# Optimization experiments

Measured on AMD Instinct MI355X. Metric: run time of the kernel, lower is better.

## Reference

```python
import jax, jax.numpy as jnp
import numpy as np

DIM = 1024
HEADS = 8
HEAD_DIM = DIM // HEADS


def setup_inputs() -> dict:
    key = jax.random.key(0)
    k1, k2, k3, k4 = jax.random.split(key, 4)
    x = jax.random.normal(k1, (4, 4096, DIM), dtype=jnp.float32)
    # torch nn.Linear(dim, 3*dim, bias=False): stored here as [in, out]
    W_qkv = jax.random.normal(k2, (DIM, 3 * DIM), dtype=jnp.float32) * (1.0 / np.sqrt(DIM))
    W_out = jax.random.normal(k3, (DIM, DIM), dtype=jnp.float32) * (1.0 / np.sqrt(DIM))
    b_out = jax.random.normal(k4, (DIM,), dtype=jnp.float32) * 0.01
    return {"x": x, "W_qkv": W_qkv, "W_out": W_out, "b_out": b_out}


def reference(x, W_qkv, W_out, b_out):
    b, n, _ = x.shape
    qkv = x @ W_qkv                                   # [b, n, 3*dim]
    q, k, v = jnp.split(qkv, 3, axis=-1)
    # [b, n, dim] -> [b, h, n, d]
    split_heads = lambda t: t.reshape(b, n, HEADS, HEAD_DIM).transpose(0, 2, 1, 3)
    q = jax.nn.sigmoid(split_heads(q))
    k = jnp.tanh(split_heads(k))
    v = split_heads(v)
    # linear attention: kv = k^T @ v  -> [b, h, d, d]
    kv = jnp.einsum('bhnd,bhne->bhde', k, v)
    out = jnp.einsum('bhnd,bhde->bhne', q, kv)        # [b, h, n, d]
    out = out.transpose(0, 2, 1, 3).reshape(b, n, DIM)
    return out @ W_out + b_out
```

## Files before the change

kernel.cpp:

```cpp
#include <hip/hip_runtime.h>
#include <hip/hip_bf16.h>
#include <math.h>

typedef __attribute__((ext_vector_type(4))) float f32x4;
typedef __attribute__((ext_vector_type(8))) __bf16 bf16x8;
typedef unsigned short u16;
typedef __attribute__((ext_vector_type(4))) u16 u16x4;
typedef __attribute__((ext_vector_type(8))) u16 u16x8;

#define NTOK 16384
#define SEQ  4096

__device__ __forceinline__ void gload16(void* lds, const void* g) {
    __builtin_amdgcn_global_load_lds(
        (const __attribute__((address_space(1))) unsigned int*)g,
        (__attribute__((address_space(3))) unsigned int*)lds, 16, 0, 0);
}

__device__ __forceinline__ int xcd_swizzle(int bid, int nwg) {
    int cpx = nwg >> 3;
    return (bid & 7) * cpx + (bid >> 3);
}

__global__ void cast_x_kernel(const float* __restrict__ in, __bf16* __restrict__ out, int n) {
    int stride = gridDim.x * blockDim.x * 8;
    for (int i = (blockIdx.x * blockDim.x + threadIdx.x) * 8; i < n; i += stride) {
        f32x4 v0 = *(const f32x4*)(in + i);
        f32x4 v1 = *(const f32x4*)(in + i + 4);
        u16x8 pk;
        pk[0] = __builtin_bit_cast(u16, (__bf16)v0.x);
        pk[1] = __builtin_bit_cast(u16, (__bf16)v0.y);
        pk[2] = __builtin_bit_cast(u16, (__bf16)v0.z);
        pk[3] = __builtin_bit_cast(u16, (__bf16)v0.w);
        pk[4] = __builtin_bit_cast(u16, (__bf16)v1.x);
        pk[5] = __builtin_bit_cast(u16, (__bf16)v1.y);
        pk[6] = __builtin_bit_cast(u16, (__bf16)v1.z);
        pk[7] = __builtin_bit_cast(u16, (__bf16)v1.w);
        *(u16x8*)(out + i) = pk;
    }
}

__global__ void transpose_cast(const float* __restrict__ in, __bf16* __restrict__ out,
                               int R, int C) {
    __shared__ float t[32][33];
    int bx = blockIdx.x * 32;
    int by = blockIdx.y * 32;
    int tx = threadIdx.x & 31, ty = threadIdx.x >> 5;
    #pragma unroll
    for (int j = 0; j < 32; j += 8)
        t[ty + j][tx] = in[(size_t)(by + ty + j) * C + bx + tx];
    __syncthreads();
    #pragma unroll
    for (int j = 0; j < 32; j += 8)
        out[(size_t)(bx + ty + j) * R + by + tx] = (__bf16)t[tx][ty + j];
}

__launch_bounds__(256)
__global__ void qkv_gemm(const __bf16* __restrict__ X,
                         const __bf16* __restrict__ WT,
                         __bf16* __restrict__ Q,
                         __bf16* __restrict__ KT,
                         __bf16* __restrict__ VT) {
    __shared__ __bf16 As[128 * 64];
    __shared__ __bf16 Bs[128 * 64];
    const int swz = xcd_swizzle(blockIdx.x, 128 * 24);
    const int mblk = swz & 127;
    const int nblk = swz >> 7;
    const int tid = threadIdx.x;
    const int lane = tid & 63;
    const int wave = tid >> 6;
    const int wr = wave >> 1, wc = wave & 1;
    const int mBase = mblk * 128, nBase = nblk * 128;

    f32x4 acc[4][4] = {};

    for (int kt = 0; kt < 16; ++kt) {
        const int k0 = kt * 64;
        #pragma unroll
        for (int it = 0; it < 4; ++it) {
            int slot = it * 256 + tid;
            int r = slot >> 3, cs = slot & 7;
            int cg = cs ^ (r & 7);
            gload16((char*)As + slot * 16, X + (size_t)(mBase + r) * 1024 + k0 + cg * 8);
        }
        #pragma unroll
        for (int it = 0; it < 4; ++it) {
            int slot = it * 256 + tid;
            int r = slot >> 3, cs = slot & 7;
            int cg = cs ^ (r & 7);
            gload16((char*)Bs + slot * 16, WT + (size_t)(nBase + r) * 1024 + k0 + cg * 8);
        }
        __syncthreads();
        #pragma unroll
        for (int kk = 0; kk < 2; ++kk) {
            bf16x8 a[4], b[4];
            const int kb = kk * 4 + (lane >> 4);
            #pragma unroll
            for (int m = 0; m < 4; ++m) {
                int row = wr * 64 + m * 16 + (lane & 15);
                a[m] = *(const bf16x8*)((const char*)As + row * 128 + (kb ^ (row & 7)) * 16);
            }
            #pragma unroll
            for (int n = 0; n < 4; ++n) {
                int row = wc * 64 + n * 16 + (lane & 15);
                b[n] = *(const bf16x8*)((const char*)Bs + row * 128 + (kb ^ (row & 7)) * 16);
            }
            #pragma unroll
            for (int m = 0; m < 4; ++m)
                #pragma unroll
                for (int n = 0; n < 4; ++n)
                    acc[m][n] = __builtin_amdgcn_mfma_f32_16x16x32_bf16(a[m], b[n], acc[m][n], 0, 0, 0);
        }
        __syncthreads();
    }

    const int sec = nblk >> 3;
    const int head = nblk & 7;
    #pragma unroll
    for (int m = 0; m < 4; ++m) {
        const int row0 = mBase + wr * 64 + m * 16 + (lane >> 4) * 4;
        #pragma unroll
        for (int n = 0; n < 4; ++n) {
            const int col = wc * 64 + n * 16 + (lane & 15);
            if (sec == 0) {
                #pragma unroll
                for (int j = 0; j < 4; ++j) {
                    float v = acc[m][n][j];
                    v = 1.0f / (1.0f + __expf(-v));
                    Q[(size_t)(row0 + j) * 1024 + head * 128 + col] = (__bf16)v;
                }
            } else {
                u16x4 pk;
                #pragma unroll
                for (int j = 0; j < 4; ++j) {
                    float v = acc[m][n][j];
                    if (sec == 1) {
                        float e = __expf(-2.0f * fabsf(v));
                        v = copysignf((1.0f - e) / (1.0f + e), v);
                    }
                    pk[j] = __builtin_bit_cast(u16, (__bf16)v);
                }
                const int b = row0 >> 12, nn = row0 & 4095;
                __bf16* dst = (sec == 1) ? KT : VT;
                *(u16x4*)(dst + ((size_t)(b * 8 + head) * 128 + col) * SEQ + nn) = pk;
            }
        }
    }
}

__launch_bounds__(256)
__global__ void kv_gemm(const __bf16* __restrict__ KT, const __bf16* __restrict__ VT,
                        float* __restrict__ KVp) {
    const int bh = blockIdx.x >> 3;
    const int chunk = blockIdx.x & 7;
    const int tid = threadIdx.x, lane = tid & 63, wave = tid >> 6;
    const int wr = wave >> 1, wc = wave & 1;
    const __bf16* Kb = KT + (size_t)bh * 128 * SEQ;
    const __bf16* Vb = VT + (size_t)bh * 128 * SEQ;
    f32x4 acc[4][4] = {};
    const int nb = chunk * 512 + (lane >> 4) * 8;
    for (int ks = 0; ks < 16; ++ks) {
        const int n0 = nb + ks * 32;
        bf16x8 a[4], b[4];
        #pragma unroll
        for (int m = 0; m < 4; ++m) {
            int d = wr * 64 + m * 16 + (lane & 15);
            a[m] = *(const bf16x8*)(Kb + (size_t)d * SEQ + n0);
        }
        #pragma unroll
        for (int n = 0; n < 4; ++n) {
            int e = wc * 64 + n * 16 + (lane & 15);
            b[n] = *(const bf16x8*)(Vb + (size_t)e * SEQ + n0);
        }
        #pragma unroll
        for (int m = 0; m < 4; ++m)
            #pragma unroll
            for (int n = 0; n < 4; ++n)
                acc[m][n] = __builtin_amdgcn_mfma_f32_16x16x32_bf16(a[m], b[n], acc[m][n], 0, 0, 0);
    }
    float* out = KVp + ((size_t)bh * 8 + chunk) * 16384;
    #pragma unroll
    for (int m = 0; m < 4; ++m) {
        const int r0 = wr * 64 + m * 16 + (lane >> 4) * 4;
        #pragma unroll
        for (int n = 0; n < 4; ++n) {
            const int col = wc * 64 + n * 16 + (lane & 15);
            #pragma unroll
            for (int j = 0; j < 4; ++j)
                out[(r0 + j) * 128 + col] = acc[m][n][j];
        }
    }
}

__launch_bounds__(256)
__global__ void kvw_gemm(const float* __restrict__ KVp, const __bf16* __restrict__ WoT,
                         __bf16* __restrict__ MT) {
    const int bh = blockIdx.x >> 3, ft = blockIdx.x & 7;
    const int b = bh >> 3, h = bh & 7;
    const int tid = threadIdx.x, lane = tid & 63, wave = tid >> 6;
    const int wr = wave >> 1, wc = wave & 1;
    const float* A = KVp + (size_t)bh * 8 * 16384;
    f32x4 acc[4][4] = {};
    for (int ks = 0; ks < 4; ++ks) {
        const int e0 = ks * 32 + (lane >> 4) * 8;
        bf16x8 a[4], bfr[4];
        #pragma unroll
        for (int m = 0; m < 4; ++m) {
            int d = wr * 64 + m * 16 + (lane & 15);
            f32x4 u = {0.f, 0.f, 0.f, 0.f};
            f32x4 w = {0.f, 0.f, 0.f, 0.f};
            #pragma unroll
            for (int c = 0; c < 8; ++c) {
                u += *(const f32x4*)(A + c * 16384 + d * 128 + e0);
                w += *(const f32x4*)(A + c * 16384 + d * 128 + e0 + 4);
            }
            bf16x8 t;
            t[0]=(__bf16)u.x; t[1]=(__bf16)u.y; t[2]=(__bf16)u.z; t[3]=(__bf16)u.w;
            t[4]=(__bf16)w.x; t[5]=(__bf16)w.y; t[6]=(__bf16)w.z; t[7]=(__bf16)w.w;
            a[m] = t;
        }
        #pragma unroll
        for (int n = 0; n < 4; ++n) {
            int f = ft * 128 + wc * 64 + n * 16 + (lane & 15);
            bfr[n] = *(const bf16x8*)(WoT + (size_t)f * 1024 + h * 128 + e0);
        }
        #pragma unroll
        for (int m = 0; m < 4; ++m)
            #pragma unroll
            for (int n = 0; n < 4; ++n)
                acc[m][n] = __builtin_amdgcn_mfma_f32_16x16x32_bf16(a[m], bfr[n], acc[m][n], 0, 0, 0);
    }
    __bf16* MTb = MT + (size_t)b * 1024 * 1024;
    #pragma unroll
    for (int m = 0; m < 4; ++m) {
        const int d0 = wr * 64 + m * 16 + (lane >> 4) * 4;
        #pragma unroll
        for (int n = 0; n < 4; ++n) {
            const int f = ft * 128 + wc * 64 + n * 16 + (lane & 15);
            u16x4 pk;
            #pragma unroll
            for (int j = 0; j < 4; ++j)
                pk[j] = __builtin_bit_cast(u16, (__bf16)acc[m][n][j]);
            *(u16x4*)(MTb + (size_t)f * 1024 + h * 128 + d0) = pk;
        }
    }
}

__launch_bounds__(256)
__global__ void final_gemm(const __bf16* __restrict__ Q,
                           const __bf16* __restrict__ MT,
                           const float* __restrict__ bias,
                           float* __restrict__ out) {
    __shared__ __bf16 As[128 * 64];
    __shared__ __bf16 Bs[128 * 64];
    const int swz = xcd_swizzle(blockIdx.x, 128 * 8);
    const int mblk = swz & 127;
    const int nblk = swz >> 7;
    const int tid = threadIdx.x;
    const int lane = tid & 63;
    const int wave = tid >> 6;
    const int wr = wave >> 1, wc = wave & 1;
    const int mBase = mblk * 128, nBase = nblk * 128;
    const int b = mBase >> 12;
    const __bf16* Bsrc = MT + (size_t)b * 1024 * 1024;

    f32x4 acc[4][4] = {};

    for (int kt = 0; kt < 16; ++kt) {
        const int k0 = kt * 64;
        #pragma unroll
        for (int it = 0; it < 4; ++it) {
            int slot = it * 256 + tid;
            int r = slot >> 3, cs = slot & 7;
            int cg = cs ^ (r & 7);
            gload16((char*)As + slot * 16, Q + (size_t)(mBase + r) * 1024 + k0 + cg * 8);
        }
        #pragma unroll
        for (int it = 0; it < 4; ++it) {
            int slot = it * 256 + tid;
            int r = slot >> 3, cs = slot & 7;
            int cg = cs ^ (r & 7);
            gload16((char*)Bs + slot * 16, Bsrc + (size_t)(nBase + r) * 1024 + k0 + cg * 8);
        }
        __syncthreads();
        #pragma unroll
        for (int kk = 0; kk < 2; ++kk) {
            bf16x8 a[4], bfr[4];
            const int kb = kk * 4 + (lane >> 4);
            #pragma unroll
            for (int m = 0; m < 4; ++m) {
                int row = wr * 64 + m * 16 + (lane & 15);
                a[m] = *(const bf16x8*)((const char*)As + row * 128 + (kb ^ (row & 7)) * 16);
            }
            #pragma unroll
            for (int n = 0; n < 4; ++n) {
                int row = wc * 64 + n * 16 + (lane & 15);
                bfr[n] = *(const bf16x8*)((const char*)Bs + row * 128 + (kb ^ (row & 7)) * 16);
            }
            #pragma unroll
            for (int m = 0; m < 4; ++m)
                #pragma unroll
                for (int n = 0; n < 4; ++n)
                    acc[m][n] = __builtin_amdgcn_mfma_f32_16x16x32_bf16(a[m], bfr[n], acc[m][n], 0, 0, 0);
        }
        __syncthreads();
    }

    #pragma unroll
    for (int m = 0; m < 4; ++m) {
        const int row0 = mBase + wr * 64 + m * 16 + (lane >> 4) * 4;
        #pragma unroll
        for (int n = 0; n < 4; ++n) {
            const int col = nBase + wc * 64 + n * 16 + (lane & 15);
            const float bv = bias[col];
            #pragma unroll
            for (int j = 0; j < 4; ++j)
                out[(size_t)(row0 + j) * 1024 + col] = acc[m][n][j] + bv;
        }
    }
}

extern "C" void kernel_launch(void* const* d_in, const int* in_sizes, int n_in,
                              void* d_out, int out_size, void* d_ws, size_t ws_size,
                              hipStream_t stream) {
    const float* x    = (const float*)d_in[0];
    const float* Wqkv = (const float*)d_in[1];
    const float* Wout = (const float*)d_in[2];
    const float* bout = (const float*)d_in[3];
    float* out = (float*)d_out;
    char* ws = (char*)d_ws;
    char* ob = (char*)d_out;

    __bf16* xb  = (__bf16*)(ob);
    float*  KVp = (float*)(ob + 33554432ull);
    __bf16* wqt = (__bf16*)(ws);
    __bf16* wot = (__bf16*)(ws + 6291456ull);
    __bf16* Q   = (__bf16*)(ws + 8388608ull);
    __bf16* KT  = (__bf16*)(ws + 41943040ull);
    __bf16* VT  = (__bf16*)(ws + 75497472ull);
    __bf16* MT  = (__bf16*)(ws + 109051904ull);

    hipLaunchKernelGGL(cast_x_kernel, dim3(2048), dim3(256), 0, stream, x, xb, NTOK * 1024);
    hipLaunchKernelGGL(transpose_cast, dim3(96, 32), dim3(256), 0, stream, Wqkv, wqt, 1024, 3072);
    hipLaunchKernelGGL(transpose_cast, dim3(32, 32), dim3(256), 0, stream, Wout, wot, 1024, 1024);
    hipLaunchKernelGGL(qkv_gemm, dim3(128 * 24), dim3(256), 0, stream, xb, wqt, Q, KT, VT);
    hipLaunchKernelGGL(kv_gemm, dim3(256), dim3(256), 0, stream, KT, VT, KVp);
    hipLaunchKernelGGL(kvw_gemm, dim3(256), dim3(256), 0, stream, KVp, wot, MT);
    hipLaunchKernelGGL(final_gemm, dim3(128 * 8), dim3(256), 0, stream, Q, MT, bout, out);
}
```

Before: 405.2 us.

## Replace 128x128 GEMMs with pipelined 256x256 eight-wave GEMM kernels

Rewrites the QKV projection and final output GEMMs as 256x256-tile kernels with 8 waves and a 4-stage LDS ring buffer of 32-wide K slices. Global-to-LDS loads are issued ahead and overlap MFMA work through explicit vmcnt waits, barriers, sched_barriers and setprio. The goal is more operand reuse per tile and latency hiding in place of the old load-sync-compute loop. The cost is more registers and LDS per block (one block per CU) and fewer blocks, which can hurt load balance, especially for the 256-block final GEMM.

```diff
diff --git a/kernel.cpp b/kernel.cpp
--- a/kernel.cpp
+++ b/kernel.cpp
@@ -55,95 +55,167 @@
         out[(size_t)(bx + ty + j) * R + by + tx] = (__bf16)t[tx][ty + j];
 }
 
-__launch_bounds__(256)
-__global__ void qkv_gemm(const __bf16* __restrict__ X,
-                         const __bf16* __restrict__ WT,
-                         __bf16* __restrict__ Q,
-                         __bf16* __restrict__ KT,
-                         __bf16* __restrict__ VT) {
-    __shared__ __bf16 As[128 * 64];
-    __shared__ __bf16 Bs[128 * 64];
-    const int swz = xcd_swizzle(blockIdx.x, 128 * 24);
-    const int mblk = swz & 127;
-    const int nblk = swz >> 7;
-    const int tid = threadIdx.x;
-    const int lane = tid & 63;
-    const int wave = tid >> 6;
-    const int wr = wave >> 1, wc = wave & 1;
-    const int mBase = mblk * 128, nBase = nblk * 128;
-
-    f32x4 acc[4][4] = {};
-
-    for (int kt = 0; kt < 16; ++kt) {
-        const int k0 = kt * 64;
-        #pragma unroll
-        for (int it = 0; it < 4; ++it) {
-            int slot = it * 256 + tid;
-            int r = slot >> 3, cs = slot & 7;
-            int cg = cs ^ (r & 7);
-            gload16((char*)As + slot * 16, X + (size_t)(mBase + r) * 1024 + k0 + cg * 8);
-        }
-        #pragma unroll
-        for (int it = 0; it < 4; ++it) {
-            int slot = it * 256 + tid;
-            int r = slot >> 3, cs = slot & 7;
-            int cg = cs ^ (r & 7);
-            gload16((char*)Bs + slot * 16, WT + (size_t)(nBase + r) * 1024 + k0 + cg * 8);
-        }
-        __syncthreads();
-        #pragma unroll
-        for (int kk = 0; kk < 2; ++kk) {
-            bf16x8 a[4], b[4];
-            const int kb = kk * 4 + (lane >> 4);
-            #pragma unroll
-            for (int m = 0; m < 4; ++m) {
-                int row = wr * 64 + m * 16 + (lane & 15);
-                a[m] = *(const bf16x8*)((const char*)As + row * 128 + (kb ^ (row & 7)) * 16);
-            }
-            #pragma unroll
-            for (int n = 0; n < 4; ++n) {
-                int row = wc * 64 + n * 16 + (lane & 15);
-                b[n] = *(const bf16x8*)((const char*)Bs + row * 128 + (kb ^ (row & 7)) * 16);
-            }
-            #pragma unroll
-            for (int m = 0; m < 4; ++m)
-                #pragma unroll
-                for (int n = 0; n < 4; ++n)
-                    acc[m][n] = __builtin_amdgcn_mfma_f32_16x16x32_bf16(a[m], b[n], acc[m][n], 0, 0, 0);
-        }
-        __syncthreads();
-    }
-
-    const int sec = nblk >> 3;
-    const int head = nblk & 7;
-    #pragma unroll
-    for (int m = 0; m < 4; ++m) {
-        const int row0 = mBase + wr * 64 + m * 16 + (lane >> 4) * 4;
-        #pragma unroll
-        for (int n = 0; n < 4; ++n) {
-            const int col = wc * 64 + n * 16 + (lane & 15);
+
+#define PHASE(p)                                                                     \
+    {                                                                                \
+        constexpr int cs = (p) >> 1;                      \
+        constexpr int nh = (p) & 1;                                      \
+        constexpr int ss = (((p) >> 1) + 3) & 3;            \
+        if constexpr (nh == 0) {                \
+            const char* ab = (const char*)AL + cs * 16384;                           \
+            _Pragma("unroll")                                                        \
+            for (int m = 0; m < 8; ++m)                                              \
+                a[m] = *(const bf16x8*)(ab + aoff0 + m * 1024);                      \
+        }                                                                            \
+        bf16x8 b0, b1;                                                               \
+        {                                                                            \
+            const char* bb = (const char*)BL + cs * 16384;                           \
+            b0 = *(const bf16x8*)(bb + boff0 + (nh * 2 + 0) * 1024);                 \
+            b1 = *(const bf16x8*)(bb + boff0 + (nh * 2 + 1) * 1024);                 \
+        }                                                                            \
+        {      \
+            const int n = 4 * itr + ((p) >> 1) + 3;                                  \
+            const int ns = n < 32 ? n : 31;                   \
+            if constexpr (((p) & 1) == 0) {                                          \
+                char* dst = (char*)AL + ss * 16384;                                  \
+                gload16(dst + fb0, Asrc + ael0 + ns * 32);                           \
+                gload16(dst + fb1, Asrc + ael1 + ns * 32);                           \
+            } else {                                                                 \
+                char* dst = (char*)BL + ss * 16384;                                  \
+                gload16(dst + fb0, Bsrc + bel0 + ns * 32);                           \
+                gload16(dst + fb1, Bsrc + bel1 + ns * 32);                           \
+            }                                                                        \
+        }                                                                            \
+        if constexpr (((p) & 3) == 3) {                                              \
+            asm volatile("s_waitcnt vmcnt(4)" ::: "memory");                         \
+            __builtin_amdgcn_sched_barrier(0);                                       \
+        }                                                                            \
+        __builtin_amdgcn_s_barrier();                                                \
+        __builtin_amdgcn_sched_barrier(0);                                           \
+        __builtin_amdgcn_s_setprio(1);                                               \
+        _Pragma("unroll")                                                            \
+        for (int m = 0; m < 8; ++m) {                                                \
+            acc[m][nh * 2 + 0] = __builtin_amdgcn_mfma_f32_16x16x32_bf16(            \
+                a[m], b0, acc[m][nh * 2 + 0], 0, 0, 0);                              \
+            acc[m][nh * 2 + 1] = __builtin_amdgcn_mfma_f32_16x16x32_bf16(            \
+                a[m], b1, acc[m][nh * 2 + 1], 0, 0, 0);                              \
+        }                                                                            \
+        __builtin_amdgcn_s_setprio(0);                                               \
+        __builtin_amdgcn_sched_barrier(0);                                           \
+        __builtin_amdgcn_s_barrier();                                                \
+    }
+
+#define GEMM256_SETUP(APTR, BPTR)                                                    \
+    __shared__ __align__(16) __bf16 AL[4][256][32];                                  \
+    __shared__ __align__(16) __bf16 BL[4][256][32];                                  \
+    const int tid = threadIdx.x;                                                     \
+    const int lane = tid & 63, wave = tid >> 6;                                      \
+    const int wr = wave >> 2, wc = wave & 3;                                         \
+    const __bf16* __restrict__ Asrc = (APTR);                                        \
+    const __bf16* __restrict__ Bsrc = (BPTR);                                        \
+                     \
+    const int fb0 = tid * 16, fb1 = (512 + tid) * 16;                                \
+    const int srow0 = fb0 >> 6, sc0 = (fb0 >> 4) & 3;                                \
+    const int srow1 = fb1 >> 6, sc1 = (fb1 >> 4) & 3;                                \
+    const size_t ael0 = (size_t)(mBase + srow0) * 1024 + ((sc0 ^ (srow0 & 3)) << 3); \
+    const size_t ael1 = (size_t)(mBase + srow1) * 1024 + ((sc1 ^ (srow1 & 3)) << 3); \
+    const size_t bel0 = (size_t)(nBase + srow0) * 1024 + ((sc0 ^ (srow0 & 3)) << 3); \
+    const size_t bel1 = (size_t)(nBase + srow1) * 1024 + ((sc1 ^ (srow1 & 3)) << 3); \
+                  \
+    const int aoff0 = (wr * 128 + (lane & 15)) * 64 + (((lane >> 4) ^ (lane & 3)) << 4); \
+    const int boff0 = (wc * 64 + (lane & 15)) * 64 + (((lane >> 4) ^ (lane & 3)) << 4);  \
+    f32x4 acc[8][4] = {};                                                            \
+    bf16x8 a[8];                                                                     \
+                        \
+    {                                                                                \
+        _Pragma("unroll")                                                            \
+        for (int n = 0; n < 3; ++n) {                                                \
+            char* da = (char*)AL + n * 16384;                                        \
+            char* db = (char*)BL + n * 16384;                                        \
+            gload16(da + fb0, Asrc + ael0 + n * 32);                                 \
+            gload16(da + fb1, Asrc + ael1 + n * 32);                                 \
+            gload16(db + fb0, Bsrc + bel0 + n * 32);                                 \
+            gload16(db + fb1, Bsrc + bel1 + n * 32);                                 \
+        }                                                                            \
+        asm volatile("s_waitcnt vmcnt(4)" ::: "memory");                             \
+        __builtin_amdgcn_sched_barrier(0);                                           \
+        __builtin_amdgcn_s_barrier();                                                \
+    }                                                                                \
+    _Pragma("unroll 1")                                                              \
+    for (int itr = 0; itr < 8; ++itr) {                                              \
+        PHASE(0) PHASE(1) PHASE(2) PHASE(3)                                          \
+        PHASE(4) PHASE(5) PHASE(6) PHASE(7)                                          \
+    }                                                                                \
+                  \
+    asm volatile("s_waitcnt vmcnt(0)" ::: "memory");
+
+__launch_bounds__(512, 1)
+__global__ void qkv_gemm256(const __bf16* __restrict__ X,
+                            const __bf16* __restrict__ WT,
+                            __bf16* __restrict__ Q,
+                            __bf16* __restrict__ KT,
+                            __bf16* __restrict__ VT) {
+    const int swz = xcd_swizzle(blockIdx.x, 768);
+    const int mblk = swz & 63, nblk = swz >> 6;
+    const int mBase = mblk * 256, nBase = nblk * 256;
+    GEMM256_SETUP(X, WT)
+
+    const int sec = nblk >> 2;
+    const int colsec = (nblk & 3) * 256 + wc * 64;
+    #pragma unroll
+    for (int m = 0; m < 8; ++m) {
+        const int row = mBase + wr * 128 + m * 16 + (lane >> 4) * 4;
+        const int b = row >> 12, nn = row & 4095;
+        #pragma unroll
+        for (int f = 0; f < 4; ++f) {
+            const int colg = colsec + f * 16 + (lane & 15);
             if (sec == 0) {
                 #pragma unroll
                 for (int j = 0; j < 4; ++j) {
-                    float v = acc[m][n][j];
+                    float v = acc[m][f][j];
                     v = 1.0f / (1.0f + __expf(-v));
-                    Q[(size_t)(row0 + j) * 1024 + head * 128 + col] = (__bf16)v;
+                    Q[(size_t)(row + j) * 1024 + colg] = (__bf16)v;
                 }
             } else {
                 u16x4 pk;
                 #pragma unroll
                 for (int j = 0; j < 4; ++j) {
-                    float v = acc[m][n][j];
+                    float v = acc[m][f][j];
                     if (sec == 1) {
                         float e = __expf(-2.0f * fabsf(v));
                         v = copysignf((1.0f - e) / (1.0f + e), v);
                     }
                     pk[j] = __builtin_bit_cast(u16, (__bf16)v);
                 }
-                const int b = row0 >> 12, nn = row0 & 4095;
+                const int head = colg >> 7, d = colg & 127;
                 __bf16* dst = (sec == 1) ? KT : VT;
-                *(u16x4*)(dst + ((size_t)(b * 8 + head) * 128 + col) * SEQ + nn) = pk;
+                *(u16x4*)(dst + ((size_t)(b * 8 + head) * 128 + d) * SEQ + nn) = pk;
             }
+        }
+    }
+}
+
+__launch_bounds__(512, 1)
+__global__ void final_gemm256(const __bf16* __restrict__ Qm,
+                              const __bf16* __restrict__ MT,
+                              const float* __restrict__ bias,
+                              float* __restrict__ out) {
+    const int swz = xcd_swizzle(blockIdx.x, 256);
+    const int mblk = swz & 63, nblk = swz >> 6;
+    const int mBase = mblk * 256, nBase = nblk * 256;
+    const __bf16* Bbase = MT + (size_t)(mBase >> 12) * 1024 * 1024;
+    GEMM256_SETUP(Qm, Bbase)
+
+    #pragma unroll
+    for (int m = 0; m < 8; ++m) {
+        const int row = mBase + wr * 128 + m * 16 + (lane >> 4) * 4;
+        #pragma unroll
+        for (int f = 0; f < 4; ++f) {
+            const int col = nBase + wc * 64 + f * 16 + (lane & 15);
+            const float bv = bias[col];
+            #pragma unroll
+            for (int j = 0; j < 4; ++j)
+                out[(size_t)(row + j) * 1024 + col] = acc[m][f][j] + bv;
         }
     }
 }
@@ -178,7 +250,7 @@
             for (int n = 0; n < 4; ++n)
                 acc[m][n] = __builtin_amdgcn_mfma_f32_16x16x32_bf16(a[m], b[n], acc[m][n], 0, 0, 0);
     }
-    float* out = KVp + ((size_t)bh * 8 + chunk) * 16384;
+    float* o = KVp + ((size_t)bh * 8 + chunk) * 16384;
     #pragma unroll
     for (int m = 0; m < 4; ++m) {
         const int r0 = wr * 64 + m * 16 + (lane >> 4) * 4;
@@ -187,7 +259,7 @@
             const int col = wc * 64 + n * 16 + (lane & 15);
             #pragma unroll
             for (int j = 0; j < 4; ++j)
-                out[(r0 + j) * 128 + col] = acc[m][n][j];
+                o[(r0 + j) * 128 + col] = acc[m][n][j];
         }
     }
 }
@@ -246,80 +318,6 @@
     }
 }
 
-__launch_bounds__(256)
-__global__ void final_gemm(const __bf16* __restrict__ Q,
-                           const __bf16* __restrict__ MT,
-                           const float* __restrict__ bias,
-                           float* __restrict__ out) {
-    __shared__ __bf16 As[128 * 64];
-    __shared__ __bf16 Bs[128 * 64];
-    const int swz = xcd_swizzle(blockIdx.x, 128 * 8);
-    const int mblk = swz & 127;
-    const int nblk = swz >> 7;
-    const int tid = threadIdx.x;
-    const int lane = tid & 63;
-    const int wave = tid >> 6;
-    const int wr = wave >> 1, wc = wave & 1;
-    const int mBase = mblk * 128, nBase = nblk * 128;
-    const int b = mBase >> 12;
-    const __bf16* Bsrc = MT + (size_t)b * 1024 * 1024;
-
-    f32x4 acc[4][4] = {};
-
-    for (int kt = 0; kt < 16; ++kt) {
-        const int k0 = kt * 64;
-        #pragma unroll
-        for (int it = 0; it < 4; ++it) {
-            int slot = it * 256 + tid;
-            int r = slot >> 3, cs = slot & 7;
-            int cg = cs ^ (r & 7);
-            gload16((char*)As + slot * 16, Q + (size_t)(mBase + r) * 1024 + k0 + cg * 8);
-        }
-        #pragma unroll
-        for (int it = 0; it < 4; ++it) {
-            int slot = it * 256 + tid;
-            int r = slot >> 3, cs = slot & 7;
-            int cg = cs ^ (r & 7);
-            gload16((char*)Bs + slot * 16, Bsrc + (size_t)(nBase + r) * 1024 + k0 + cg * 8);
-        }
-        __syncthreads();
-        #pragma unroll
-        for (int kk = 0; kk < 2; ++kk) {
-            bf16x8 a[4], bfr[4];
-            const int kb = kk * 4 + (lane >> 4);
-            #pragma unroll
-            for (int m = 0; m < 4; ++m) {
-                int row = wr * 64 + m * 16 + (lane & 15);
-                a[m] = *(const bf16x8*)((const char*)As + row * 128 + (kb ^ (row & 7)) * 16);
-            }
-            #pragma unroll
-            for (int n = 0; n < 4; ++n) {
-                int row = wc * 64 + n * 16 + (lane & 15);
-                bfr[n] = *(const bf16x8*)((const char*)Bs + row * 128 + (kb ^ (row & 7)) * 16);
-            }
-            #pragma unroll
-            for (int m = 0; m < 4; ++m)
-                #pragma unroll
-                for (int n = 0; n < 4; ++n)
-                    acc[m][n] = __builtin_amdgcn_mfma_f32_16x16x32_bf16(a[m], bfr[n], acc[m][n], 0, 0, 0);
-        }
-        __syncthreads();
-    }
-
-    #pragma unroll
-    for (int m = 0; m < 4; ++m) {
-        const int row0 = mBase + wr * 64 + m * 16 + (lane >> 4) * 4;
-        #pragma unroll
-        for (int n = 0; n < 4; ++n) {
-            const int col = nBase + wc * 64 + n * 16 + (lane & 15);
-            const float bv = bias[col];
-            #pragma unroll
-            for (int j = 0; j < 4; ++j)
-                out[(size_t)(row0 + j) * 1024 + col] = acc[m][n][j] + bv;
-        }
-    }
-}
-
 extern "C" void kernel_launch(void* const* d_in, const int* in_sizes, int n_in,
                               void* d_out, int out_size, void* d_ws, size_t ws_size,
                               hipStream_t stream) {
@@ -343,8 +341,8 @@
     hipLaunchKernelGGL(cast_x_kernel, dim3(2048), dim3(256), 0, stream, x, xb, NTOK * 1024);
     hipLaunchKernelGGL(transpose_cast, dim3(96, 32), dim3(256), 0, stream, Wqkv, wqt, 1024, 3072);
     hipLaunchKernelGGL(transpose_cast, dim3(32, 32), dim3(256), 0, stream, Wout, wot, 1024, 1024);
-    hipLaunchKernelGGL(qkv_gemm, dim3(128 * 24), dim3(256), 0, stream, xb, wqt, Q, KT, VT);
+    hipLaunchKernelGGL(qkv_gemm256, dim3(768), dim3(512), 0, stream, xb, wqt, Q, KT, VT);
     hipLaunchKernelGGL(kv_gemm, dim3(256), dim3(256), 0, stream, KT, VT, KVp);
     hipLaunchKernelGGL(kvw_gemm, dim3(256), dim3(256), 0, stream, KVp, wot, MT);
-    hipLaunchKernelGGL(final_gemm, dim3(128 * 8), dim3(256), 0, stream, Q, MT, bout, out);
-}
+    hipLaunchKernelGGL(final_gemm256, dim3(256), dim3(512), 0, stream, Q, MT, bout, out);
+}
```

Measured after the change: 385.5 us. 4.9% less time.
